# Optimization experiments

Hardware: AMD Instinct MI355X
Metric: run time of the kernel (lower is better)

Reference implementation:

```python
import jax, jax.numpy as jnp
import numpy as np

N = 20000      # nodes
E = 320000     # edges (before self loops)
HID = 128      # args.hidden
HEADS = 8
C1 = HID // 2  # 64, gat1 out per head -> 512 concat
C2 = HID // 4  # 32, gat2 out per head -> 256 concat
D1 = HEADS * C1  # 512
D2 = HEADS * C2  # 256
JKD = HID + D1 + D2  # 896


def _glorot(key, shape):
    fan_in, fan_out = shape[0], shape[-1]
    s = jnp.sqrt(6.0 / (fan_in + fan_out))
    return jax.random.uniform(key, shape, jnp.float32, -s, s)


def setup_inputs() -> dict:
    key = jax.random.key(0)
    ks = jax.random.split(key, 18)
    x = jax.random.normal(ks[0], (N, HID), jnp.float32)
    edge_index = jax.random.randint(ks[1], (2, E), 0, N, dtype=jnp.int32)
    return {
        "x": x,
        "edge_index": edge_index,
        # GATv2 layer 1
        "Wl1": _glorot(ks[2], (HID, D1)), "bl1": jnp.zeros((D1,), jnp.float32),
        "Wr1": _glorot(ks[3], (HID, D1)), "br1": jnp.zeros((D1,), jnp.float32),
        "att1": _glorot(ks[4], (HEADS, C1)),
        "bias1": jnp.zeros((D1,), jnp.float32),
        # GATv2 layer 2
        "Wl2": _glorot(ks[5], (D1, D2)), "bl2": jnp.zeros((D2,), jnp.float32),
        "Wr2": _glorot(ks[6], (D1, D2)), "br2": jnp.zeros((D2,), jnp.float32),
        "att2": _glorot(ks[7], (HEADS, C2)),
        "bias2": jnp.zeros((D2,), jnp.float32),
        # JK linear
        "Wjk": _glorot(ks[8], (JKD, HID)), "bjk": jnp.zeros((HID,), jnp.float32),
    }


def gatv2_layer(x, src, dst, Wl, bl, Wr, br, att, bias, n):
    """PyG GATv2Conv (concat=True, eval mode: no dropout), neg_slope=0.2."""
    H, C = att.shape
    xl = (x @ Wl + bl).reshape(n, H, C)  # source transform (messages)
    xr = (x @ Wr + br).reshape(n, H, C)  # target transform
    e = jax.nn.leaky_relu(xl[src] + xr[dst], 0.2)        # [E,H,C]
    logits = jnp.einsum('ehc,hc->eh', e, att)            # [E,H]
    # numerically stable segment softmax over incoming edges per dst node
    m = jax.ops.segment_max(logits, dst, num_segments=n) # [N,H]
    a = jnp.exp(logits - m[dst])
    denom = jax.ops.segment_sum(a, dst, num_segments=n)
    alpha = a / denom[dst]                               # [E,H]
    out = jax.ops.segment_sum(alpha[:, :, None] * xl[src], dst, num_segments=n)
    return out.reshape(n, H * C) + bias


def reference(x, edge_index, Wl1, bl1, Wr1, br1, att1, bias1,
              Wl2, bl2, Wr2, br2, att2, bias2, Wjk, bjk):
    n = x.shape[0]
    loop = jnp.arange(n, dtype=edge_index.dtype)
    src = jnp.concatenate([edge_index[0], loop])  # add self loops (PyG default)
    dst = jnp.concatenate([edge_index[1], loop])

    jk0 = x
    h1 = jax.nn.elu(gatv2_layer(x, src, dst, Wl1, bl1, Wr1, br1, att1, bias1, n))
    h2 = jax.nn.elu(gatv2_layer(h1, src, dst, Wl2, bl2, Wr2, br2, att2, bias2, n))
    jk = jnp.concatenate([jk0, h1, h2], axis=-1)  # JumpingKnowledge('cat')
    return jk @ Wjk + bjk
```

## Files before the change

kernel.cpp:

```cpp
#include <hip/hip_runtime.h>

typedef unsigned short u16;
typedef __attribute__((ext_vector_type(8))) short bf16x8;
typedef __attribute__((ext_vector_type(4))) float f32x4;

__device__ __forceinline__ float bf2f(u16 u) { return __uint_as_float(((unsigned)u) << 16); }
__device__ __forceinline__ u16 f2bf(float f) {
  unsigned u = __float_as_uint(f);
  u += 0x7fffu + ((u >> 16) & 1u);
  return (u16)(u >> 16);
}
__device__ __forceinline__ void bf2x2(unsigned w, float& lo, float& hi) {
  lo = __uint_as_float(w << 16);
  hi = __uint_as_float(w & 0xffff0000u);
}
__device__ __forceinline__ unsigned pk2(float lo, float hi) {
  return (unsigned)f2bf(lo) | ((unsigned)f2bf(hi) << 16);
}

__device__ __forceinline__ float red8(float p) {
  p += __int_as_float(__builtin_amdgcn_ds_swizzle(__float_as_int(p), 0x041F));
  p += __int_as_float(__builtin_amdgcn_ds_swizzle(__float_as_int(p), 0x081F));
  p += __int_as_float(__builtin_amdgcn_ds_swizzle(__float_as_int(p), 0x101F));
  return p;
}
__device__ __forceinline__ float red4(float p) {
  p += __int_as_float(__builtin_amdgcn_ds_swizzle(__float_as_int(p), 0x041F));
  p += __int_as_float(__builtin_amdgcn_ds_swizzle(__float_as_int(p), 0x081F));
  return p;
}

__global__ __launch_bounds__(256) void prepw_kernel(
    const float* __restrict__ x,
    const float* __restrict__ bl1, const float* __restrict__ br1,
    const float* __restrict__ bl2, const float* __restrict__ br2,
    const float* __restrict__ Wl1, const float* __restrict__ Wr1,
    const float* __restrict__ Wl2, const float* __restrict__ Wr2,
    const float* __restrict__ Wjk,
    u16* __restrict__ XH, float* __restrict__ BC1, float* __restrict__ BC2,
    int* __restrict__ cur, u16* __restrict__ Wp,
    int nx, int total, int prepBlocks)
{
  if (blockIdx.x < prepBlocks) {
    int i = blockIdx.x * 256 + threadIdx.x;
    if (i >= total) return;
    if (i < nx) { XH[i] = f2bf(x[i]); return; }
    int j = i - nx;
    if (j < 1024) { BC1[j] = (j < 512) ? bl1[j] : br1[j - 512]; return; }
    if (j < 1536) { int t = j - 1024; BC2[t] = (t < 256) ? bl2[t] : br2[t - 256]; return; }
    cur[j - 1536] = 0;
    return;
  }
  __shared__ float T[64][65];
  int t = blockIdx.x - prepBlocks;
  const float *Wa, *Wb; int Nhalf, lds, k0, n0, KsT, SUBS; size_t obase; bool split;
  if (t < 32) {
    int kt = t & 1, nt = t >> 1;
    k0 = kt * 64; n0 = nt * 64; obase = 0; KsT = 4; SUBS = 8; split = true;
    Wa = Wl1; Wb = Wr1; Nhalf = 512; lds = 512;
  } else if (t < 96) {
    int tt = t - 32; int kt = tt & 7, nt = tt >> 3;
    k0 = kt * 64; n0 = nt * 64; obase = 262144; KsT = 16; SUBS = 8; split = true;
    Wa = Wl2; Wb = Wr2; Nhalf = 256; lds = 256;
  } else {
    int tt = t - 96; int kt = tt % 14, nt = tt / 14;
    k0 = kt * 64; n0 = nt * 64; obase = 786432; KsT = 28; SUBS = 4; split = false;
    Wa = Wjk; Wb = nullptr; Nhalf = 128; lds = 128;
  }
  const int tid = threadIdx.x;
  const int lane = tid & 63, unit = tid >> 6;
  {
    int n = n0 + lane;
    const float* S = (n < Nhalf) ? Wa : Wb;
    int nn = (n < Nhalf) ? n : n - Nhalf;
#pragma unroll
    for (int r = 0; r < 16; ++r) {
      int kl = unit + 4 * r;
      T[kl][lane] = S[(size_t)(k0 + kl) * lds + nn];
    }
  }
  __syncthreads();
  const int tn = n0 >> 6;
#pragma unroll
  for (int u = 0; u < 2; ++u) {
    int c = unit * 2 + u;
    int ks_l = c >> 2, nc = c & 3;
    int ksg = (k0 >> 5) + ks_l;
    size_t ob = obase + ((size_t)(tn * KsT + ksg) * SUBS + nc) * 512 + lane * 8;
#pragma unroll
    for (int j = 0; j < 8; ++j) {
      float v = T[ks_l * 32 + (lane >> 4) * 8 + j][nc * 16 + (lane & 15)];
      u16 h = f2bf(v);
      Wp[ob + j] = h;
      if (split) Wp[ob + 2048 + j] = f2bf(v - bf2f(h));
    }
  }
}

__global__ __launch_bounds__(256) void hist_kernel(
    const int* __restrict__ ei, int E, int ET, int* __restrict__ cnt)
{
  int e = blockIdx.x * 256 + threadIdx.x;
  if (e >= ET) return;
  int d = (e < E) ? ei[E + e] : (e - E);
  atomicAdd(&cnt[d], 1);
}

__global__ __launch_bounds__(1024) void scan_kernel(
    int* __restrict__ cnt, int* __restrict__ rowptr, int* __restrict__ perm,
    int n)
{
  __shared__ int wsum[16];
  __shared__ int carry;
  __shared__ int dh[64];
  __shared__ int dbase[64];
  const int tid = threadIdx.x, lane = tid & 63, wv = tid >> 6;
  if (tid == 0) carry = 0;
  if (tid < 64) dh[tid] = 0;
  __syncthreads();
  for (int base = 0; base < n; base += 1024) {
    int i = base + tid;
    int v = (i < n) ? cnt[i] : 0;
    if (i < n) {
      cnt[i] = 0;
      atomicAdd(&dh[v < 63 ? v : 63], 1);
    }
    int s = v;
#pragma unroll
    for (int ofs = 1; ofs < 64; ofs <<= 1) {
      int t = __shfl_up(s, ofs);
      if (lane >= ofs) s += t;
    }
    if (lane == 63) wsum[wv] = s;
    __syncthreads();
    if (wv == 0 && lane < 16) {
      int t = wsum[lane];
#pragma unroll
      for (int ofs = 1; ofs < 16; ofs <<= 1) {
        int u = __shfl_up(t, ofs);
        if (lane >= ofs) t += u;
      }
      wsum[lane] = t;
    }
    __syncthreads();
    int waveoff = (wv == 0) ? 0 : wsum[wv - 1];
    if (i < n) rowptr[i] = carry + waveoff + s - v;
    int tot = wsum[15];
    __syncthreads();
    if (tid == 0) carry += tot;
    __syncthreads();
  }
  if (tid == 0) rowptr[n] = carry;
  __syncthreads();
  if (tid == 0) {
    int s = 0;
    for (int k = 63; k >= 0; --k) { dbase[k] = s; s += dh[k]; }
  }
  __syncthreads();
  if (tid < 64) dh[tid] = 0;
  __syncthreads();
  for (int base = 0; base < n; base += 1024) {
    int i = base + tid;
    if (i < n) {
      int deg = rowptr[i + 1] - rowptr[i];
      int b = deg < 63 ? deg : 63;
      int pos = dbase[b] + atomicAdd(&dh[b], 1);
      perm[pos] = i;
    }
  }
}

template<int MROWS, int NW, bool SPLIT, bool BF16OUT>
__device__ __forceinline__ void gemmct_body(
    u16* __restrict__ ldsA, int bid,
    const u16* __restrict__ A0, int lda0, int K0,
    const u16* __restrict__ A1, int lda1, int K1,
    const u16* __restrict__ A2, int lda2, int K2,
    const u16* __restrict__ Wp, int KsT,
    int kof0, int kof1, int kof2,
    const float* __restrict__ bias,
    void* __restrict__ Cv, int ldc, int M, int N)
{
  constexpr int SUBS = SPLIT ? 8 : 4;
  const int tid  = threadIdx.x;
  const int lane = tid & 63;
  const int wv   = tid >> 6;
  const int quad = lane >> 4;
  const int r16  = lane & 15;
  const int m0   = bid * MROWS;

  const u16* As[3]   = {A0, A1, A2};
  const int  Ks[3]   = {K0, K1, K2};
  const int  ldas[3] = {lda0, lda1, lda2};
  const int  kofs[3] = {kof0, kof1, kof2};

  int soff[3];
  int so = 0;
#pragma unroll
  for (int s = 0; s < 3; ++s) {
    const int K = Ks[s];
    soff[s] = so;
    if (K == 0) continue;
    const int stride = K + 8;
    const int cpr = K >> 3;
    const int sh  = 32 - __clz(cpr - 1);
    const int tot = MROWS << sh;
    for (int c = tid; c < tot; c += NW * 64) {
      int row = c >> sh, kc = c & ((1 << sh) - 1);
      if (kc < cpr) {
        int sr = m0 + row; if (sr >= M) sr = M - 1;
        uint4 v = *reinterpret_cast<const uint4*>(As[s] + (size_t)sr * ldas[s] + kc * 8);
        *reinterpret_cast<uint4*>(&ldsA[so + row * stride + kc * 8]) = v;
      }
    }
    so += MROWS * stride;
  }
  __syncthreads();

  constexpr int MM = MROWS / 16;
  for (int n0w = wv * 64; n0w < N; n0w += NW * 64) {
    const int t = n0w >> 6;
    f32x4 acc[MM][4];
#pragma unroll
    for (int mm = 0; mm < MM; ++mm)
#pragma unroll
      for (int nc = 0; nc < 4; ++nc) acc[mm][nc] = (f32x4){0.f, 0.f, 0.f, 0.f};

#pragma unroll
    for (int s = 0; s < 3; ++s) {
      const int K = Ks[s];
      if (K == 0) continue;
      const int stride = K + 8;
      const int ksb = kofs[s] >> 5;
      const u16* lbase = &ldsA[soff[s] + r16 * stride + quad * 8];

#pragma unroll 2
      for (int k0 = 0; k0 < K; k0 += 32) {
        const int ks = ksb + (k0 >> 5);
        const u16* ch = Wp + (((size_t)(t * KsT + ks) * SUBS) << 9) + lane * 8;
        bf16x8 af[MM];
#pragma unroll
        for (int mm = 0; mm < MM; ++mm)
          af[mm] = *reinterpret_cast<const bf16x8*>(lbase + mm * 16 * stride + k0);
        bf16x8 whf[4], wlf[4];
#pragma unroll
        for (int nc = 0; nc < 4; ++nc) {
          whf[nc] = *reinterpret_cast<const bf16x8*>(ch + (nc << 9));
          if (SPLIT) wlf[nc] = *reinterpret_cast<const bf16x8*>(ch + ((4 + nc) << 9));
        }
#pragma unroll
        for (int mm = 0; mm < MM; ++mm)
#pragma unroll
          for (int nc = 0; nc < 4; ++nc) {
            acc[mm][nc] = __builtin_amdgcn_mfma_f32_16x16x32_bf16(whf[nc], af[mm], acc[mm][nc], 0, 0, 0);
            if (SPLIT)
              acc[mm][nc] = __builtin_amdgcn_mfma_f32_16x16x32_bf16(wlf[nc], af[mm], acc[mm][nc], 0, 0, 0);
          }
      }
    }

#pragma unroll
    for (int mm = 0; mm < MM; ++mm) {
      const int m = m0 + mm * 16 + r16;
      if (m >= M) continue;
#pragma unroll
      for (int nc = 0; nc < 4; ++nc) {
        const int n = n0w + nc * 16 + quad * 4;
        float b0 = 0.f, b1 = 0.f, b2 = 0.f, b3 = 0.f;
        if (bias) {
          float4 bv = *reinterpret_cast<const float4*>(bias + n);
          b0 = bv.x; b1 = bv.y; b2 = bv.z; b3 = bv.w;
        }
        float v0 = acc[mm][nc][0] + b0;
        float v1 = acc[mm][nc][1] + b1;
        float v2 = acc[mm][nc][2] + b2;
        float v3 = acc[mm][nc][3] + b3;
        if (BF16OUT) {
          ushort4 o = { f2bf(v0), f2bf(v1), f2bf(v2), f2bf(v3) };
          *reinterpret_cast<ushort4*>((u16*)Cv + (size_t)m * ldc + n) = o;
        } else {
          float4 o = { v0, v1, v2, v3 };
          *reinterpret_cast<float4*>((float*)Cv + (size_t)m * ldc + n) = o;
        }
      }
    }
  }
}

template<int MROWS, int NW, int WPE, bool SPLIT, bool BF16OUT, int LDSU16>
__global__ __launch_bounds__(NW * 64, WPE) void gemmct_kernel(
    const u16* __restrict__ A0, int lda0, int K0,
    const u16* __restrict__ A1, int lda1, int K1,
    const u16* __restrict__ A2, int lda2, int K2,
    const u16* __restrict__ Wp, int KsT,
    int kof0, int kof1, int kof2,
    const float* __restrict__ bias,
    void* __restrict__ Cv, int ldc, int M, int N)
{
  __shared__ u16 ldsA[LDSU16];
  gemmct_body<MROWS, NW, SPLIT, BF16OUT>(
      ldsA, blockIdx.x, A0, lda0, K0, A1, lda1, K1, A2, lda2, K2,
      Wp, KsT, kof0, kof1, kof2, bias, Cv, ldc, M, N);
}

template<int MROWS, int NW, int WPE, bool SPLIT, bool BF16OUT, int LDSU16>
__global__ __launch_bounds__(NW * 64, WPE) void gemm1_scatter_kernel(
    const u16* __restrict__ A0, int lda0, int K0,
    const u16* __restrict__ Wp, int KsT,
    const float* __restrict__ bias,
    void* __restrict__ Cv, int ldc, int M, int N, int gemmBlocks,
    const int* __restrict__ ei, int E, int ET,
    const int* __restrict__ rowptr, int* __restrict__ cur, int* __restrict__ srcs)
{
  __shared__ u16 ldsA[LDSU16];
  if ((int)blockIdx.x < gemmBlocks) {
    gemmct_body<MROWS, NW, SPLIT, BF16OUT>(
        ldsA, blockIdx.x, A0, lda0, K0, nullptr, 0, 0, nullptr, 0, 0,
        Wp, KsT, 0, 0, 0, bias, Cv, ldc, M, N);
    return;
  }
  int e = ((int)blockIdx.x - gemmBlocks) * (NW * 64) + (int)threadIdx.x;
  if (e >= ET) return;
  int s, d;
  if (e < E) { s = ei[e]; d = ei[E + e]; } else { s = e - E; d = s; }
  int pos = rowptr[d] + atomicAdd(&cur[d], 1);
  srcs[pos] = s;
}

template<int VPL>
__device__ __forceinline__ void load_row(const u16* p, float* dst) {
  if constexpr (VPL == 8) {
    uint4 t = *reinterpret_cast<const uint4*>(p);
    bf2x2(t.x, dst[0], dst[1]); bf2x2(t.y, dst[2], dst[3]);
    bf2x2(t.z, dst[4], dst[5]); bf2x2(t.w, dst[6], dst[7]);
  } else {
    uint2 t = *reinterpret_cast<const uint2*>(p);
    bf2x2(t.x, dst[0], dst[1]); bf2x2(t.y, dst[2], dst[3]);
  }
}

__global__ __launch_bounds__(256) void gath1_kernel(
    const u16* __restrict__ XLR,
    const int* __restrict__ rowptr, const int* __restrict__ srcs,
    const int* __restrict__ perm,
    const float* __restrict__ att, const float* __restrict__ bias,
    u16* __restrict__ Hh, int Nn)
{
  const int tid   = threadIdx.x;
  const int s     = tid & 7;
  const int gib   = tid >> 3;
  const int head  = blockIdx.x & 7;
  const int chunk = blockIdx.x >> 3;

  const int idx = chunk * 32 + gib;
  if (idx >= Nn) return;
  const int d = perm[idx];

  const int hoff = head * 64 + s * 8;

  float c1[8], c2[8], biasR[8];
#pragma unroll
  for (int w = 0; w < 8; ++w) {
    float a = att[hoff + w];
    c1[w] = 0.6f * a;
    c2[w] = 0.4f * a;
    biasR[w] = bias[hoff + w];
  }

  float xr[8];
  load_row<8>(XLR + (size_t)d * 1024 + 512 + hoff, xr);
  const int jb = rowptr[d], je = rowptr[d + 1];

  float acc[8];
  load_row<8>(XLR + (size_t)srcs[jb] * 1024 + hoff, acc);
  float p0 = 0.f;
#pragma unroll
  for (int w = 0; w < 8; ++w) {
    float v = acc[w] + xr[w];
    p0 = fmaf(c1[w], v, fmaf(c2[w], fabsf(v), p0));
  }
  p0 = red8(p0);
  float den = 1.f;

  int j = jb + 1;
  for (; j + 1 < je; j += 2) {
    float xa[8], xb[8];
    load_row<8>(XLR + (size_t)srcs[j]     * 1024 + hoff, xa);
    load_row<8>(XLR + (size_t)srcs[j + 1] * 1024 + hoff, xb);
    float pa = 0.f, pb = 0.f;
#pragma unroll
    for (int w = 0; w < 8; ++w) {
      float va = xa[w] + xr[w];
      float vb = xb[w] + xr[w];
      pa = fmaf(c1[w], va, fmaf(c2[w], fabsf(va), pa));
      pb = fmaf(c1[w], vb, fmaf(c2[w], fabsf(vb), pb));
    }
    pa = red8(pa); pb = red8(pb);
    const float ea = __expf(pa - p0);
    const float eb = __expf(pb - p0);
    den += ea + eb;
#pragma unroll
    for (int w = 0; w < 8; ++w)
      acc[w] = fmaf(ea, xa[w], fmaf(eb, xb[w], acc[w]));
  }
  if (j < je) {
    float xa[8];
    load_row<8>(XLR + (size_t)srcs[j] * 1024 + hoff, xa);
    float pa = 0.f;
#pragma unroll
    for (int w = 0; w < 8; ++w) {
      float va = xa[w] + xr[w];
      pa = fmaf(c1[w], va, fmaf(c2[w], fabsf(va), pa));
    }
    pa = red8(pa);
    const float ea = __expf(pa - p0);
    den += ea;
#pragma unroll
    for (int w = 0; w < 8; ++w) acc[w] = fmaf(ea, xa[w], acc[w]);
  }

  const float inv = 1.f / den;
  float o[8];
#pragma unroll
  for (int w = 0; w < 8; ++w) {
    float v = fmaf(acc[w], inv, biasR[w]);
    o[w] = v > 0.f ? v : (__expf(v) - 1.f);
  }
  uint4 ov = { pk2(o[0], o[1]), pk2(o[2], o[3]), pk2(o[4], o[5]), pk2(o[6], o[7]) };
  *reinterpret_cast<uint4*>(Hh + (size_t)d * 512 + hoff) = ov;
}

__global__ __launch_bounds__(256) void gath2_kernel(
    const u16* __restrict__ XLR,
    const int* __restrict__ rowptr, const int* __restrict__ srcs,
    const int* __restrict__ perm,
    const float* __restrict__ att, const float* __restrict__ bias,
    u16* __restrict__ Hh, int Nn)
{
  const int tid   = threadIdx.x;
  const int s     = tid & 3;
  const int gib   = tid >> 2;
  const int head  = blockIdx.x & 7;
  const int chunk = blockIdx.x >> 3;

  const int idx = chunk * 64 + gib;
  if (idx >= Nn) return;
  const int d = perm[idx];

  const int hoff = head * 32 + s * 8;

  float c1[8], c2[8], biasR[8];
#pragma unroll
  for (int w = 0; w < 8; ++w) {
    float a = att[hoff + w];
    c1[w] = 0.6f * a;
    c2[w] = 0.4f * a;
    biasR[w] = bias[hoff + w];
  }

  float xr[8];
  load_row<8>(XLR + (size_t)d * 512 + 256 + hoff, xr);
  const int jb = rowptr[d], je = rowptr[d + 1];

  float acc[8];
  load_row<8>(XLR + (size_t)srcs[jb] * 512 + hoff, acc);
  float p0 = 0.f;
#pragma unroll
  for (int w = 0; w < 8; ++w) {
    float v = acc[w] + xr[w];
    p0 = fmaf(c1[w], v, fmaf(c2[w], fabsf(v), p0));
  }
  p0 = red4(p0);
  float den = 1.f;

  int j = jb + 1;
  for (; j + 1 < je; j += 2) {
    float xa[8], xb[8];
    load_row<8>(XLR + (size_t)srcs[j]     * 512 + hoff, xa);
    load_row<8>(XLR + (size_t)srcs[j + 1] * 512 + hoff, xb);
    float pa = 0.f, pb = 0.f;
#pragma unroll
    for (int w = 0; w < 8; ++w) {
      float va = xa[w] + xr[w];
      float vb = xb[w] + xr[w];
      pa = fmaf(c1[w], va, fmaf(c2[w], fabsf(va), pa));
      pb = fmaf(c1[w], vb, fmaf(c2[w], fabsf(vb), pb));
    }
    pa = red4(pa); pb = red4(pb);
    const float ea = __expf(pa - p0);
    const float eb = __expf(pb - p0);
    den += ea + eb;
#pragma unroll
    for (int w = 0; w < 8; ++w)
      acc[w] = fmaf(ea, xa[w], fmaf(eb, xb[w], acc[w]));
  }
  if (j < je) {
    float xa[8];
    load_row<8>(XLR + (size_t)srcs[j] * 512 + hoff, xa);
    float pa = 0.f;
#pragma unroll
    for (int w = 0; w < 8; ++w) {
      float va = xa[w] + xr[w];
      pa = fmaf(c1[w], va, fmaf(c2[w], fabsf(va), pa));
    }
    pa = red4(pa);
    const float ea = __expf(pa - p0);
    den += ea;
#pragma unroll
    for (int w = 0; w < 8; ++w) acc[w] = fmaf(ea, xa[w], acc[w]);
  }

  const float inv = 1.f / den;
  float o[8];
#pragma unroll
  for (int w = 0; w < 8; ++w) {
    float v = fmaf(acc[w], inv, biasR[w]);
    o[w] = v > 0.f ? v : (__expf(v) - 1.f);
  }
  uint4 ov = { pk2(o[0], o[1]), pk2(o[2], o[3]), pk2(o[4], o[5]), pk2(o[6], o[7]) };
  *reinterpret_cast<uint4*>(Hh + (size_t)d * 256 + hoff) = ov;
}


extern "C" void kernel_launch(void* const* d_in, const int* in_sizes, int n_in,
                              void* d_out, int out_size, void* d_ws, size_t ws_size,
                              hipStream_t stream) {
  const float* x     = (const float*)d_in[0];
  const int*   ei    = (const int*)d_in[1];
  const float* Wl1   = (const float*)d_in[2];
  const float* bl1   = (const float*)d_in[3];
  const float* Wr1   = (const float*)d_in[4];
  const float* br1   = (const float*)d_in[5];
  const float* att1  = (const float*)d_in[6];
  const float* bias1 = (const float*)d_in[7];
  const float* Wl2   = (const float*)d_in[8];
  const float* bl2   = (const float*)d_in[9];
  const float* Wr2   = (const float*)d_in[10];
  const float* br2   = (const float*)d_in[11];
  const float* att2  = (const float*)d_in[12];
  const float* bias2 = (const float*)d_in[13];
  const float* Wjk   = (const float*)d_in[14];
  const float* bjk   = (const float*)d_in[15];
  float* out = (float*)d_out;

  const int Nn = in_sizes[0] / 128;
  const int E  = in_sizes[1] / 2;
  const int ET = E + Nn;

  const size_t nx = (size_t)Nn * 128;

  const size_t oW1  = 0;
  const size_t oW2  = 262144;
  const size_t oWjk = 786432;
  const size_t npack = 901120;

  char* ws = (char*)d_ws;
  size_t off = 0;
  u16* XH = (u16*)(ws + off); off += nx * 2;
  u16* Wp = (u16*)(ws + off); off += npack * 2;
  float* BC1 = (float*)(ws + off); off += 1024 * 4;
  float* BC2 = (float*)(ws + off); off += 512 * 4;
  u16* XLR1 = (u16*)(ws + off);
  u16* XLR2 = XLR1;
  off += (size_t)Nn * 1024 * 2;
  u16* H1h = (u16*)(ws + off); off += (size_t)Nn * 512 * 2;
  u16* H2h = (u16*)(ws + off); off += (size_t)Nn * 256 * 2;
  int* rowptr = (int*)(ws + off); off += (size_t)(Nn + 1) * 4;
  int* cur    = (int*)(ws + off); off += (size_t)Nn * 4;
  int* perm   = (int*)(ws + off); off += (size_t)Nn * 4;
  int* srcs   = (int*)(ws + off); off += (size_t)ET * 4;

  const int nprep = (int)(nx + 1536 + Nn);
  const int prepBlocks = (nprep + 255) / 256;
  prepw_kernel<<<prepBlocks + 124, 256, 0, stream>>>(
      x, bl1, br1, bl2, br2, Wl1, Wr1, Wl2, Wr2, Wjk,
      XH, BC1, BC2, cur, Wp, (int)nx, nprep, prepBlocks);
  hist_kernel<<<(ET + 255) / 256, 256, 0, stream>>>(ei, E, ET, cur);
  scan_kernel<<<1, 1024, 0, stream>>>(cur, rowptr, perm, Nn);

  const int g1blocks = (Nn + 31) / 32;
  const int scatBlocks = (ET + 511) / 512;
  gemm1_scatter_kernel<32, 8, 4, true, true, 32 * 136>
      <<<g1blocks + scatBlocks, 512, 0, stream>>>(
      XH, 128, 128,
      Wp + oW1, 4, BC1,
      XLR1, 1024, Nn, 1024, g1blocks,
      ei, E, ET, rowptr, cur, srcs);
  gath1_kernel<<<5000, 256, 0, stream>>>(
      XLR1, rowptr, srcs, perm, att1, bias1, H1h, Nn);

  gemmct_kernel<48, 8, 4, true, true, 48 * 520>
      <<<(Nn + 47) / 48, 512, 0, stream>>>(
      H1h, 512, 512, nullptr, 0, 0, nullptr, 0, 0,
      Wp + oW2, 16, 0, 0, 0, BC2,
      XLR2, 512, Nn, 512);
  gath2_kernel<<<2504, 256, 0, stream>>>(
      XLR2, rowptr, srcs, perm, att2, bias2, H2h, Nn);

  gemmct_kernel<16, 2, 1, false, false, 16 * 920>
      <<<(Nn + 15) / 16, 128, 0, stream>>>(
      XH, 128, 128, H1h, 512, 512, H2h, 256, 256,
      Wp + oWjk, 28, 0, 128, 640, bjk,
      out, 128, Nn, 128);
}
```

Measured before the change: 300.3 us.

## Chunk serial scan per thread and move degree-bucket permutation into scatter kernel

The single-block scan now processes 20 consecutive counts per thread, which cuts the number of serial 1024-wide iterations and block barriers. The degree-sorted permutation that used to run at the end of that single block is moved into extra blocks of the gemm1/scatter launch, with bucket bases and counters kept in global memory. This takes serial single-block work off the critical path at the cost of global atomics on 64 bucket counters and strided per-thread loads in the scan.

```diff
diff --git a/kernel.cpp b/kernel.cpp
--- a/kernel.cpp
+++ b/kernel.cpp
@@ -107,25 +107,34 @@
 }
 
 __global__ __launch_bounds__(1024) void scan_kernel(
-    int* __restrict__ cnt, int* __restrict__ rowptr, int* __restrict__ perm,
-    int n)
-{
+    int* __restrict__ cnt, int* __restrict__ rowptr,
+    int* __restrict__ dbaseG, int* __restrict__ dcntG, int n)
+{
+  constexpr int CH = 20;
   __shared__ int wsum[16];
-  __shared__ int carry;
   __shared__ int dh[64];
-  __shared__ int dbase[64];
+  __shared__ int carrysh;
   const int tid = threadIdx.x, lane = tid & 63, wv = tid >> 6;
-  if (tid == 0) carry = 0;
   if (tid < 64) dh[tid] = 0;
+  if (tid == 0) carrysh = 0;
   __syncthreads();
-  for (int base = 0; base < n; base += 1024) {
-    int i = base + tid;
-    int v = (i < n) ? cnt[i] : 0;
-    if (i < n) {
-      cnt[i] = 0;
-      atomicAdd(&dh[v < 63 ? v : 63], 1);
-    }
-    int s = v;
+
+  for (int base = 0; base < n; base += 1024 * CH) {
+    const int i0 = base + tid * CH;
+    int v[CH];
+    int run = 0;
+#pragma unroll
+    for (int j = 0; j < CH; ++j) {
+      int i = i0 + j;
+      int c = (i < n) ? cnt[i] : 0;
+      v[j] = c;
+      run += c;
+      if (i < n) {
+        cnt[i] = 0;
+        atomicAdd(&dh[c < 63 ? c : 63], 1);
+      }
+    }
+    int s = run;
 #pragma unroll
     for (int ofs = 1; ofs < 64; ofs <<= 1) {
       int t = __shfl_up(s, ofs);
@@ -143,31 +152,25 @@
       wsum[lane] = t;
     }
     __syncthreads();
-    int waveoff = (wv == 0) ? 0 : wsum[wv - 1];
-    if (i < n) rowptr[i] = carry + waveoff + s - v;
+    int e = carrysh + ((wv == 0) ? 0 : wsum[wv - 1]) + s - run;
+#pragma unroll
+    for (int j = 0; j < CH; ++j) {
+      int i = i0 + j;
+      if (i < n) rowptr[i] = e;
+      e += v[j];
+    }
     int tot = wsum[15];
     __syncthreads();
-    if (tid == 0) carry += tot;
+    if (tid == 0) carrysh += tot;
     __syncthreads();
   }
-  if (tid == 0) rowptr[n] = carry;
+  if (tid == 0) rowptr[n] = carrysh;
   __syncthreads();
   if (tid == 0) {
-    int s = 0;
-    for (int k = 63; k >= 0; --k) { dbase[k] = s; s += dh[k]; }
-  }
-  __syncthreads();
-  if (tid < 64) dh[tid] = 0;
-  __syncthreads();
-  for (int base = 0; base < n; base += 1024) {
-    int i = base + tid;
-    if (i < n) {
-      int deg = rowptr[i + 1] - rowptr[i];
-      int b = deg < 63 ? deg : 63;
-      int pos = dbase[b] + atomicAdd(&dh[b], 1);
-      perm[pos] = i;
-    }
-  }
+    int acc = 0;
+    for (int k = 63; k >= 0; --k) { dbaseG[k] = acc; acc += dh[k]; }
+  }
+  if (tid < 64) dcntG[tid] = 0;
 }
 
 template<int MROWS, int NW, bool SPLIT, bool BF16OUT>
@@ -309,8 +312,10 @@
     const u16* __restrict__ Wp, int KsT,
     const float* __restrict__ bias,
     void* __restrict__ Cv, int ldc, int M, int N, int gemmBlocks,
-    const int* __restrict__ ei, int E, int ET,
-    const int* __restrict__ rowptr, int* __restrict__ cur, int* __restrict__ srcs)
+    const int* __restrict__ ei, int E, int ET, int scatBlocks,
+    const int* __restrict__ rowptr, int* __restrict__ cur, int* __restrict__ srcs,
+    const int* __restrict__ dbaseG, int* __restrict__ dcntG,
+    int* __restrict__ perm, int Nn)
 {
   __shared__ u16 ldsA[LDSU16];
   if ((int)blockIdx.x < gemmBlocks) {
@@ -319,12 +324,22 @@
         Wp, KsT, 0, 0, 0, bias, Cv, ldc, M, N);
     return;
   }
-  int e = ((int)blockIdx.x - gemmBlocks) * (NW * 64) + (int)threadIdx.x;
-  if (e >= ET) return;
-  int s, d;
-  if (e < E) { s = ei[e]; d = ei[E + e]; } else { s = e - E; d = s; }
-  int pos = rowptr[d] + atomicAdd(&cur[d], 1);
-  srcs[pos] = s;
+  int bb = (int)blockIdx.x - gemmBlocks;
+  if (bb < scatBlocks) {
+    int e = bb * (NW * 64) + (int)threadIdx.x;
+    if (e >= ET) return;
+    int s, d;
+    if (e < E) { s = ei[e]; d = ei[E + e]; } else { s = e - E; d = s; }
+    int pos = rowptr[d] + atomicAdd(&cur[d], 1);
+    srcs[pos] = s;
+    return;
+  }
+  int i = (bb - scatBlocks) * (NW * 64) + (int)threadIdx.x;
+  if (i >= Nn) return;
+  int deg = rowptr[i + 1] - rowptr[i];
+  int b = deg < 63 ? deg : 63;
+  int pos = dbaseG[b] + atomicAdd(&dcntG[b], 1);
+  perm[pos] = i;
 }
 
 template<int VPL>
@@ -568,6 +583,8 @@
   int* rowptr = (int*)(ws + off); off += (size_t)(Nn + 1) * 4;
   int* cur    = (int*)(ws + off); off += (size_t)Nn * 4;
   int* perm   = (int*)(ws + off); off += (size_t)Nn * 4;
+  int* dbaseG = (int*)(ws + off); off += 64 * 4;
+  int* dcntG  = (int*)(ws + off); off += 64 * 4;
   int* srcs   = (int*)(ws + off); off += (size_t)ET * 4;
 
   const int nprep = (int)(nx + 1536 + Nn);
@@ -576,16 +593,18 @@
       x, bl1, br1, bl2, br2, Wl1, Wr1, Wl2, Wr2, Wjk,
       XH, BC1, BC2, cur, Wp, (int)nx, nprep, prepBlocks);
   hist_kernel<<<(ET + 255) / 256, 256, 0, stream>>>(ei, E, ET, cur);
-  scan_kernel<<<1, 1024, 0, stream>>>(cur, rowptr, perm, Nn);
+  scan_kernel<<<1, 1024, 0, stream>>>(cur, rowptr, dbaseG, dcntG, Nn);
 
   const int g1blocks = (Nn + 31) / 32;
   const int scatBlocks = (ET + 511) / 512;
+  const int permBlocks = (Nn + 511) / 512;
   gemm1_scatter_kernel<32, 8, 4, true, true, 32 * 136>
-      <<<g1blocks + scatBlocks, 512, 0, stream>>>(
+      <<<g1blocks + scatBlocks + permBlocks, 512, 0, stream>>>(
       XH, 128, 128,
       Wp + oW1, 4, BC1,
       XLR1, 1024, Nn, 1024, g1blocks,
-      ei, E, ET, rowptr, cur, srcs);
+      ei, E, ET, scatBlocks, rowptr, cur, srcs,
+      dbaseG, dcntG, perm, Nn);
   gath1_kernel<<<5000, 256, 0, stream>>>(
       XLR1, rowptr, srcs, perm, att1, bias1, H1h, Nn);
 
```

Result: slower. 353.8 us (+17.8%).
